# Kernel optimization log

Measured on AMD Instinct MI355X. Metric: run time of the kernel, lower is better.

The kernel has to match this reference:

```python
import jax, jax.numpy as jnp
import numpy as np

MODEL_DIM = 2048
N_HEADS = 16
T_MAX = 2048
LATENT = 512
DHR = 64
DK = MODEL_DIM // N_HEADS  # 128
B = 4
T = 2048


def _rope_tables(t, d):
    # pos pattern [0,0,1,1,...] matching repeat(2).reshape in source
    pos = jnp.repeat(jnp.arange(d // 2, dtype=jnp.float32), 2)
    theta = jnp.power(10000.0, -2.0 * pos / d)  # (d,)
    freq = jnp.arange(t, dtype=jnp.float32)[:, None]  # (t,1)
    ang = freq * theta[None, :]  # (t,d)
    return jnp.cos(ang), jnp.sin(ang)


def _apply_rope(x, cos, sin):
    # x: (B, nh, T, d); interleaved rotate-half: (x1,x2) -> (-x2, x1)
    b, nh, t, d = x.shape
    x2 = x.reshape(b, nh, t, d // 2, 2)
    x_rot = jnp.stack([-x2[..., 1], x2[..., 0]], axis=-1).reshape(b, nh, t, d)
    return x * cos[None, None] + x_rot * sin[None, None]


def setup_inputs() -> dict:
    key = jax.random.key(0)
    ks = jax.random.split(key, 14)
    s = 0.02
    f32 = jnp.float32
    return {
        "x": jax.random.normal(ks[0], (B, T, MODEL_DIM), dtype=f32),
        "W_down": jax.random.normal(ks[1], (MODEL_DIM, 2 * LATENT), dtype=f32) * s,
        "b_down": jnp.zeros((2 * LATENT,), dtype=f32),
        "W_uKV": jax.random.normal(ks[2], (LATENT, 2 * MODEL_DIM), dtype=f32) * s,
        "b_uKV": jnp.zeros((2 * MODEL_DIM,), dtype=f32),
        "W_uQ": jax.random.normal(ks[3], (LATENT, MODEL_DIM), dtype=f32) * s,
        "b_uQ": jnp.zeros((MODEL_DIM,), dtype=f32),
        "W_kr": jax.random.normal(ks[4], (MODEL_DIM, DHR), dtype=f32) * s,
        "b_kr": jnp.zeros((DHR,), dtype=f32),
        "W_qr": jax.random.normal(ks[5], (MODEL_DIM, DHR * N_HEADS), dtype=f32) * s,
        "b_qr": jnp.zeros((DHR * N_HEADS,), dtype=f32),
        "W_out": jax.random.normal(ks[6], (MODEL_DIM, MODEL_DIM), dtype=f32) * s,
        "b_out": jnp.zeros((MODEL_DIM,), dtype=f32),
    }


def reference(x, W_down, b_down, W_uKV, b_uKV, W_uQ, b_uQ,
              W_kr, b_kr, W_qr, b_qr, W_out, b_out):
    b, t, c = x.shape
    cos, sin = _rope_tables(T_MAX, DHR)
    cos, sin = cos[:t], sin[:t]

    # low-rank down projection -> latent for KV and latent for Q
    down = x @ W_down + b_down  # (B,T,2*LATENT)
    cKV, cq = jnp.split(down, 2, axis=-1)

    # decoupled RoPE channels
    kR = _apply_rope((x @ W_kr + b_kr)[:, None], cos, sin)  # (B,1,T,dhR)
    kR = jnp.broadcast_to(kR, (b, N_HEADS, t, DHR))
    qR = (x @ W_qr + b_qr).reshape(b, t, N_HEADS, DHR).transpose(0, 2, 1, 3)
    qR = _apply_rope(qR, cos, sin)  # (B,nh,T,dhR)

    # up-projections
    v_k = (cKV @ W_uKV + b_uKV).reshape(b, t, N_HEADS, 2 * DK).transpose(0, 2, 1, 3)
    v, k = jnp.split(v_k, 2, axis=-1)  # (B,nh,T,dk) each
    k = jnp.concatenate([k, kR], axis=-1)  # (B,nh,T,dk+dhR)
    q = (cq @ W_uQ + b_uQ).reshape(b, t, N_HEADS, DK).transpose(0, 2, 1, 3)
    q = jnp.concatenate([q, qR], axis=-1)  # (B,nh,T,dk+dhR)

    # scaled dot-product attention (unmasked, as in source; scale uses dk only)
    w = jnp.einsum('bhtd,bhsd->bhts', q, k) * (1.0 / DK ** 0.5)
    w = jax.nn.softmax(w, axis=-1)
    out = jnp.einsum('bhts,bhsd->bhtd', w, v)  # (B,nh,T,dk)
    out = out.transpose(0, 2, 1, 3).reshape(b, t, MODEL_DIM)
    return out @ W_out + b_out
```

## Files before the change

kernel.cpp:

```cpp
#include <hip/hip_runtime.h>
#include <hip/hip_bf16.h>

typedef unsigned short u16;
typedef unsigned int u32;
typedef __attribute__((ext_vector_type(4))) float f32x4;
typedef __attribute__((ext_vector_type(8))) short s16x8;

#define NHEADS 16
#define TSEQ 2048
#define BATCH 4
#define BT (BATCH*TSEQ)

__device__ __forceinline__ float bf2f(u16 v){ u32 u=((u32)v)<<16; return __builtin_bit_cast(float,u); }
__device__ __forceinline__ u16 f2bf(float f){ u32 u=__builtin_bit_cast(u32,f); u += 0x7fffu + ((u>>16)&1u); return (u16)(u>>16); }

__device__ __forceinline__ void gload16(const void* g, void* l){
  __builtin_amdgcn_global_load_lds((const __attribute__((address_space(1))) u32*)g,
                                   (__attribute__((address_space(3))) u32*)l, 16, 0, 0);
}

__global__ void cast_bf16_kernel(const float* __restrict__ in, u16* __restrict__ out, long n){
  long i = ((long)blockIdx.x*256 + threadIdx.x)*4;
  if (i >= n) return;
  float4 v = *(const float4*)(in + i);
  ushort4 o;
  o.x = f2bf(v.x); o.y = f2bf(v.y); o.z = f2bf(v.z); o.w = f2bf(v.w);
  *(ushort4*)(out + i) = o;
}

__global__ void transpose_cast_kernel(const float* __restrict__ in, u16* __restrict__ out, int R, int C){
  __shared__ float tile[32][33];
  int bc = blockIdx.x*32, br = blockIdx.y*32;
  int lx = threadIdx.x & 31, ly = threadIdx.x >> 5;
  #pragma unroll
  for (int i=0;i<32;i+=8)
    tile[ly+i][lx] = in[(long)(br+ly+i)*C + bc + lx];
  __syncthreads();
  #pragma unroll
  for (int i=0;i<32;i+=8)
    out[(long)(bc+ly+i)*R + br + lx] = f2bf(tile[lx][ly+i]);
}

__global__ void rope_tab_kernel(float* __restrict__ ctab, float* __restrict__ stab){
  int idx = blockIdx.x*256 + threadIdx.x;
  int t = idx >> 5, i = idx & 31;
  float theta = expf(-(float)i * (9.210340371976184f/32.0f));
  float ang = (float)t * theta;
  float s, c;
  sincosf(ang, &s, &c);
  ctab[idx] = c; stab[idx] = s;
}

__global__ void concat_bias_kernel(const float* __restrict__ a, const float* __restrict__ b,
                                   const float* __restrict__ c, float* __restrict__ o){
  int i = blockIdx.x*256 + threadIdx.x;
  if (i >= 2176) return;
  float v = 0.f;
  if (i < 1024) v = a[i];
  else if (i < 2048) v = b[i-1024];
  else if (i < 2112) v = c[i-2048];
  o[i] = v;
}

__global__ void rope_inplace_kernel(u32* __restrict__ buf, const float* __restrict__ ct,
                                    const float* __restrict__ st, int log2ppr, int rstride){
  long idx = (long)blockIdx.x*256 + threadIdx.x;
  long row = idx >> log2ppr;
  int pp = (int)(idx & ((1<<log2ppr)-1));
  int t = (int)(row & (TSEQ-1));
  int pr = pp & 31;
  u32* p = buf + row*(long)rstride + pp;
  u32 v = *p;
  float x0 = bf2f((u16)v), x1 = bf2f((u16)(v>>16));
  float c = ct[t*32+pr], s = st[t*32+pr];
  float y0 = x0*c - x1*s;
  float y1 = x1*c + x0*s;
  *p = (u32)f2bf(y0) | ((u32)f2bf(y1)<<16);
}

template<int OUTF32>
__global__ __launch_bounds__(256,2) void gemm_bt_kernel(
    const u16* __restrict__ A, const u16* __restrict__ Bt, const float* __restrict__ bias,
    void* __restrict__ Cp, int M, int N, int K, int lda, int ldb, int ldc)
{
  __shared__ u16 As[128*32];
  __shared__ u16 Bs[128*32];
  const int tid = threadIdx.x;
  const int lane = tid & 63;
  const int wave = tid >> 6;
  const long bm = (long)blockIdx.x * 128;
  const long bn = (long)blockIdx.y * 128;
  const int wr = (wave>>1)*64, wc = (wave&1)*64;
  const int g = lane>>4, r15 = lane&15;

  f32x4 acc[4][4];
  #pragma unroll
  for (int m=0;m<4;m++)
    #pragma unroll
    for (int n=0;n<4;n++) acc[m][n] = (f32x4){0.f,0.f,0.f,0.f};

  const int c0 = tid, c1 = tid + 256;
  const u16* gA0 = A + (bm + (c0>>2))*lda + (c0&3)*8;
  const u16* gA1 = A + (bm + (c1>>2))*lda + (c1&3)*8;
  const u16* gB0 = Bt + (bn + (c0>>2))*ldb + (c0&3)*8;
  const u16* gB1 = Bt + (bn + (c1>>2))*ldb + (c1&3)*8;
  u16* lA0 = As + c0*8;
  u16* lA1 = As + c1*8;
  u16* lB0 = Bs + c0*8;
  u16* lB1 = Bs + c1*8;

  for (int k0 = 0; k0 < K; k0 += 32) {
    __syncthreads();
    gload16(gA0 + k0, lA0);
    gload16(gA1 + k0, lA1);
    gload16(gB0 + k0, lB0);
    gload16(gB1 + k0, lB1);
    __syncthreads();
    s16x8 af[4], bfr[4];
    #pragma unroll
    for (int m=0;m<4;m++) af[m] = *(const s16x8*)(As + (wr + m*16 + r15)*32 + g*8);
    #pragma unroll
    for (int n=0;n<4;n++) bfr[n] = *(const s16x8*)(Bs + (wc + n*16 + r15)*32 + g*8);
    #pragma unroll
    for (int m=0;m<4;m++)
      #pragma unroll
      for (int n=0;n<4;n++)
        acc[m][n] = __builtin_amdgcn_mfma_f32_16x16x32_bf16(af[m], bfr[n], acc[m][n], 0,0,0);
  }

  #pragma unroll
  for (int n=0;n<4;n++){
    long col = bn + wc + n*16 + r15;
    if (col >= N) continue;
    float bv = bias[col];
    #pragma unroll
    for (int m=0;m<4;m++){
      long row0 = bm + wr + m*16 + g*4;
      #pragma unroll
      for (int i=0;i<4;i++){
        long row = row0 + i;
        if (row < M){
          float v = acc[m][n][i] + bv;
          if (OUTF32) ((float*)Cp)[row*(long)ldc + col] = v;
          else        ((u16*)Cp)[row*(long)ldc + col] = f2bf(v);
        }
      }
    }
  }
}

__global__ void transpose_v_kernel(const u16* __restrict__ vk_b, u16* __restrict__ Vt){
  __shared__ u16 tile[128][130];
  int t0 = blockIdx.x*128;
  int bh = blockIdx.y;
  int b = bh>>4, h = bh&15;
  for (int idx = threadIdx.x; idx < 128*128; idx += 256){
    int r = idx>>7, c = idx&127;
    tile[r][c] = vk_b[((long)(b*TSEQ + t0 + r))*4096 + h*256 + c];
  }
  __syncthreads();
  for (int idx = threadIdx.x; idx < 128*128; idx += 256){
    int d = idx>>7, tt = idx&127;
    Vt[((long)bh*128 + d)*TSEQ + t0 + tt] = tile[tt][d];
  }
}

__global__ __launch_bounds__(256,2) void attn_kernel(
    const u16* __restrict__ q_b, const u16* __restrict__ qrB,
    const u16* __restrict__ vk_b, const u16* __restrict__ krB,
    const u16* __restrict__ Vt, u16* __restrict__ attn_b)
{
  __shared__ u16 Ks[64*192];
  __shared__ u16 Vs[128*64];
  __shared__ u16 Ps[4][16*64];

  const int tid = threadIdx.x;
  const int lane = tid & 63;
  const int wave = tid >> 6;
  const int g = lane >> 4;
  const int r15 = lane & 15;
  const int bh = blockIdx.y;
  const int b = bh>>4, h = bh&15;
  const int q0 = blockIdx.x*64 + wave*16;

  s16x8 qf[6];
  {
    const u16* qp  = q_b + ((long)b*TSEQ + q0 + r15)*2048 + h*128 + g*8;
    const u16* qrp = qrB + ((long)b*TSEQ + q0 + r15)*2112 + h*64  + g*8;
    #pragma unroll
    for (int kd=0;kd<4;kd++) qf[kd] = *(const s16x8*)(qp + kd*32);
    qf[4] = *(const s16x8*)(qrp);
    qf[5] = *(const s16x8*)(qrp + 32);
  }

  f32x4 oacc[8];
  #pragma unroll
  for (int i=0;i<8;i++) oacc[i] = (f32x4){0.f,0.f,0.f,0.f};
  float mrow[4] = {-__builtin_inff(),-__builtin_inff(),-__builtin_inff(),-__builtin_inff()};
  float lrow[4] = {0.f,0.f,0.f,0.f};

  const int krow_s = tid>>2;
  const int kslot_s = tid&3;
  const int vrow_s = tid>>1;
  const int vslot_s = tid&1;
  const u16* kbase = vk_b + (long)b*TSEQ*4096 + h*256 + 128 + kslot_s*8;
  const u16* rbase = krB + (long)b*TSEQ*2112 + kslot_s*8;
  const long vg_base = (long)bh*128*TSEQ;
  char* KsB = (char*)Ks;
  char* VsB = (char*)Vs;
  char* PsB = (char*)(&Ps[wave][0]);

  s16x8 kreg[6], vreg[4];

  auto load_regs = [&](int kt){
    long t = (long)(kt*64 + krow_s);
    const u16* kp = kbase + t*4096;
    const u16* rp = rbase + t*2112;
    #pragma unroll
    for (int j=0;j<4;j++) kreg[j] = *(const s16x8*)(kp + j*32);
    kreg[4] = *(const s16x8*)(rp);
    kreg[5] = *(const s16x8*)(rp + 32);
    const u16* vsrc = Vt + vg_base + (long)vrow_s*TSEQ + kt*64 + vslot_s*8;
    #pragma unroll
    for (int j=0;j<4;j++) vreg[j] = *(const s16x8*)(vsrc + j*16);
  };
  auto write_lds = [&](){
    u32 base = (u32)((krow_s*24 + kslot_s)*16);
    u32 sw = (u32)((krow_s&7)<<4);
    #pragma unroll
    for (int j=0;j<6;j++)
      *(s16x8*)(KsB + ((base + j*64) ^ sw)) = kreg[j];
    u32 vbase = (u32)((vrow_s*8 + vslot_s)*16);
    u32 vsw = (u32)((vrow_s&7)<<4);
    #pragma unroll
    for (int j=0;j<4;j++)
      *(s16x8*)(VsB + ((vbase + j*32) ^ vsw)) = vreg[j];
  };

  load_regs(0);
  write_lds();
  __syncthreads();

  for (int kt=0; kt<32; ++kt) {
    if (kt < 31) load_regs(kt+1);

    f32x4 sacc[4];
    #pragma unroll
    for (int n=0;n<4;n++) sacc[n] = (f32x4){0.f,0.f,0.f,0.f};
    __builtin_amdgcn_s_setprio(1);
    #pragma unroll
    for (int kd=0; kd<6; kd++){
      #pragma unroll
      for (int n=0;n<4;n++){
        int krow = n*16 + r15;
        u32 byt = (u32)(krow*384 + kd*64 + g*16) ^ (u32)((krow&7)<<4);
        s16x8 kfr = *(const s16x8*)(KsB + byt);
        sacc[n] = __builtin_amdgcn_mfma_f32_16x16x32_bf16(qf[kd], kfr, sacc[n], 0,0,0);
      }
    }
    __builtin_amdgcn_s_setprio(0);

    const float scale = 0.08838834764831845f;
    float tmax[4];
    #pragma unroll
    for (int i=0;i<4;i++){
      float m0 = fmaxf(fmaxf(sacc[0][i],sacc[1][i]), fmaxf(sacc[2][i],sacc[3][i]));
      #pragma unroll
      for (int off=1; off<16; off<<=1) m0 = fmaxf(m0, __shfl_xor(m0, off));
      tmax[i] = m0*scale;
    }
    float grow = 0.f;
    #pragma unroll
    for (int i=0;i<4;i++) grow = fmaxf(grow, tmax[i]-mrow[i]);
    if (__any(grow > 8.0f)){
      float psc[4];
      #pragma unroll
      for (int i=0;i<4;i++){
        float mn = fmaxf(mrow[i], tmax[i]);
        psc[i] = __expf(mrow[i]-mn);
        mrow[i] = mn;
        lrow[i] *= psc[i];
      }
      #pragma unroll
      for (int nf=0;nf<8;nf++){
        f32x4 o = oacc[nf];
        o[0]*=psc[0]; o[1]*=psc[1]; o[2]*=psc[2]; o[3]*=psc[3];
        oacc[nf] = o;
      }
    }
    float rs[4] = {0.f,0.f,0.f,0.f};
    #pragma unroll
    for (int n=0;n<4;n++){
      #pragma unroll
      for (int i=0;i<4;i++){
        float p = __expf(sacc[n][i]*scale - mrow[i]);
        rs[i] += p;
        int prow = g*4+i;
        u32 pb = (u32)(prow*128 + (n*16+r15)*2) ^ (u32)((prow&7)<<4);
        *(u16*)(PsB + pb) = f2bf(p);
      }
    }
    #pragma unroll
    for (int i=0;i<4;i++){
      float rsum = rs[i];
      #pragma unroll
      for (int off=1; off<16; off<<=1) rsum += __shfl_xor(rsum, off);
      lrow[i] += rsum;
    }

    __builtin_amdgcn_s_setprio(1);
    #pragma unroll
    for (int ks=0; ks<2; ks++){
      u32 pb = (u32)(r15*128 + ks*64 + g*16) ^ (u32)((r15&7)<<4);
      s16x8 pf = *(const s16x8*)(PsB + pb);
      #pragma unroll
      for (int nf=0;nf<8;nf++){
        int vrow = nf*16 + r15;
        u32 vb = (u32)(vrow*128 + ks*64 + g*16) ^ (u32)((vrow&7)<<4);
        s16x8 vf = *(const s16x8*)(VsB + vb);
        oacc[nf] = __builtin_amdgcn_mfma_f32_16x16x32_bf16(pf, vf, oacc[nf], 0,0,0);
      }
    }
    __builtin_amdgcn_s_setprio(0);

    __syncthreads();
    if (kt < 31) write_lds();
    __syncthreads();
  }

  #pragma unroll
  for (int nf=0;nf<8;nf++){
    #pragma unroll
    for (int i=0;i<4;i++){
      float v = oacc[nf][i] / lrow[i];
      long t = q0 + g*4 + i;
      attn_b[((long)b*TSEQ + t)*2048 + h*128 + nf*16 + r15] = f2bf(v);
    }
  }
}

extern "C" void kernel_launch(void* const* d_in, const int* in_sizes, int n_in,
                              void* d_out, int out_size, void* d_ws, size_t ws_size,
                              hipStream_t stream)
{
  const float* x      = (const float*)d_in[0];
  const float* W_down = (const float*)d_in[1];
  const float* b_down = (const float*)d_in[2];
  const float* W_uKV  = (const float*)d_in[3];
  const float* b_uKV  = (const float*)d_in[4];
  const float* W_uQ   = (const float*)d_in[5];
  const float* b_uQ   = (const float*)d_in[6];
  const float* W_kr   = (const float*)d_in[7];
  const float* b_kr   = (const float*)d_in[8];
  const float* W_qr   = (const float*)d_in[9];
  const float* b_qr   = (const float*)d_in[10];
  const float* W_out  = (const float*)d_in[11];
  const float* b_out  = (const float*)d_in[12];
  float* out = (float*)d_out;

  char* ws = (char*)d_ws;
  size_t off = 0;
  auto alloc = [&](size_t b)->char* { char* p = ws + off; off += (b + 255) & ~(size_t)255; return p; };

  u16* xb     = (u16*)alloc((size_t)BT*2048*2);
  u16* attn_b = xb;
  u16* q_b    = (u16*)alloc((size_t)BT*2048*2);
  u16* vk_b   = (u16*)alloc((size_t)BT*4096*2);
  u16* C1     = (u16*)alloc((size_t)BT*2112*2);
  u16* W1_t   = (u16*)alloc((size_t)2176*2048*2);
  u16* WuKV_t = (u16*)alloc((size_t)4096*512*2);
  u16* WuQ_t  = (u16*)alloc((size_t)2048*512*2);
  u16* Wout_t = (u16*)alloc((size_t)2048*2048*2);
  float* ctab = (float*)alloc((size_t)2048*32*4);
  float* stab = (float*)alloc((size_t)2048*32*4);
  float* bias1= (float*)alloc((size_t)2176*4);
  u16* Vt     = (u16*)d_out;

  long nx = (long)BT*2048;
  cast_bf16_kernel<<<dim3((u32)(nx/4/256)), 256, 0, stream>>>(x, xb, nx);
  transpose_cast_kernel<<<dim3(32, 64), 256, 0, stream>>>(W_down, W1_t,             2048, 1024);
  transpose_cast_kernel<<<dim3(32, 64), 256, 0, stream>>>(W_qr,  W1_t + 1024*2048,  2048, 1024);
  transpose_cast_kernel<<<dim3(2, 64),  256, 0, stream>>>(W_kr,  W1_t + 2048*2048,  2048, 64);
  transpose_cast_kernel<<<dim3(128,16), 256, 0, stream>>>(W_uKV, WuKV_t, 512, 4096);
  transpose_cast_kernel<<<dim3(64, 16), 256, 0, stream>>>(W_uQ,  WuQ_t, 512, 2048);
  transpose_cast_kernel<<<dim3(64, 64), 256, 0, stream>>>(W_out, Wout_t, 2048, 2048);
  rope_tab_kernel<<<dim3(256), 256, 0, stream>>>(ctab, stab);
  concat_bias_kernel<<<dim3(9), 256, 0, stream>>>(b_down, b_qr, b_kr, bias1);

  gemm_bt_kernel<0><<<dim3(64, 17), 256, 0, stream>>>(xb, W1_t, bias1, C1, 8192, 2112, 2048, 2048, 2048, 2112);
  gemm_bt_kernel<0><<<dim3(64, 32), 256, 0, stream>>>(C1,       WuKV_t, b_uKV, vk_b, 8192, 4096, 512, 2112, 512, 4096);
  gemm_bt_kernel<0><<<dim3(64, 16), 256, 0, stream>>>(C1 + 512, WuQ_t,  b_uQ,  q_b,  8192, 2048, 512, 2112, 512, 2048);

  rope_inplace_kernel<<<dim3(16384), 256, 0, stream>>>((u32*)(C1 + 1024), ctab, stab, 9, 1056);
  rope_inplace_kernel<<<dim3(1024),  256, 0, stream>>>((u32*)(C1 + 2048), ctab, stab, 5, 1056);
  transpose_v_kernel<<<dim3(16, 64), 256, 0, stream>>>(vk_b, Vt);

  attn_kernel<<<dim3(32, 64), 256, 0, stream>>>(q_b, C1 + 1024, vk_b, C1 + 2048, Vt, attn_b);

  gemm_bt_kernel<1><<<dim3(64, 16), 256, 0, stream>>>(attn_b, Wout_t, b_out, out, 8192, 2048, 2048, 2048, 2048, 2048);
}
```

Before: 900.7 us.

## Switch attention to 32x32x16 MFMA with 32-row query tiles per wave

The attention kernel now uses 32x32x16 bf16 MFMA instead of 16x16x32, and each wave handles 32 query rows instead of 16. The block therefore covers 128 queries and the grid is halved. This halves K/V tile reloads from global and LDS per query and gives fewer, larger MFMA issues. The cost is more registers (16-row softmax state, f32x16 accumulators), which may reduce occupancy under launch_bounds(256,2), and the grid is halved to 1024 blocks.

```diff
diff --git a/kernel.cpp b/kernel.cpp
--- a/kernel.cpp
+++ b/kernel.cpp
@@ -4,6 +4,7 @@
 typedef unsigned short u16;
 typedef unsigned int u32;
 typedef __attribute__((ext_vector_type(4))) float f32x4;
+typedef __attribute__((ext_vector_type(16))) float f32x16;
 typedef __attribute__((ext_vector_type(8))) short s16x8;
 
 #define NHEADS 16
@@ -172,32 +173,35 @@
 {
   __shared__ u16 Ks[64*192];
   __shared__ u16 Vs[128*64];
-  __shared__ u16 Ps[4][16*64];
+  __shared__ u16 Ps[4][32*64];
 
   const int tid = threadIdx.x;
   const int lane = tid & 63;
   const int wave = tid >> 6;
-  const int g = lane >> 4;
-  const int r15 = lane & 15;
+  const int hi = lane >> 5;
+  const int r31 = lane & 31;
   const int bh = blockIdx.y;
   const int b = bh>>4, h = bh&15;
-  const int q0 = blockIdx.x*64 + wave*16;
-
-  s16x8 qf[6];
+  const int q0 = blockIdx.x*128 + wave*32;
+
+  s16x8 qf[12];
   {
-    const u16* qp  = q_b + ((long)b*TSEQ + q0 + r15)*2048 + h*128 + g*8;
-    const u16* qrp = qrB + ((long)b*TSEQ + q0 + r15)*2112 + h*64  + g*8;
-    #pragma unroll
-    for (int kd=0;kd<4;kd++) qf[kd] = *(const s16x8*)(qp + kd*32);
-    qf[4] = *(const s16x8*)(qrp);
-    qf[5] = *(const s16x8*)(qrp + 32);
-  }
-
-  f32x4 oacc[8];
-  #pragma unroll
-  for (int i=0;i<8;i++) oacc[i] = (f32x4){0.f,0.f,0.f,0.f};
-  float mrow[4] = {-__builtin_inff(),-__builtin_inff(),-__builtin_inff(),-__builtin_inff()};
-  float lrow[4] = {0.f,0.f,0.f,0.f};
+    const u16* qp  = q_b + ((long)b*TSEQ + q0 + r31)*2048 + h*128 + hi*8;
+    const u16* qrp = qrB + ((long)b*TSEQ + q0 + r31)*2112 + h*64  + hi*8;
+    #pragma unroll
+    for (int kd=0;kd<8;kd++)  qf[kd] = *(const s16x8*)(qp + kd*16);
+    #pragma unroll
+    for (int kd=8;kd<12;kd++) qf[kd] = *(const s16x8*)(qrp + (kd-8)*16);
+  }
+
+  f32x16 oacc[4];
+  #pragma unroll
+  for (int n=0;n<4;n++)
+    #pragma unroll
+    for (int r=0;r<16;r++) oacc[n][r] = 0.f;
+  float mrow[16], lrow[16];
+  #pragma unroll
+  for (int r=0;r<16;r++){ mrow[r] = -__builtin_inff(); lrow[r] = 0.f; }
 
   const int krow_s = tid>>2;
   const int kslot_s = tid&3;
@@ -244,81 +248,78 @@
   for (int kt=0; kt<32; ++kt) {
     if (kt < 31) load_regs(kt+1);
 
-    f32x4 sacc[4];
-    #pragma unroll
-    for (int n=0;n<4;n++) sacc[n] = (f32x4){0.f,0.f,0.f,0.f};
+    f32x16 sacc0, sacc1;
+    #pragma unroll
+    for (int r=0;r<16;r++){ sacc0[r]=0.f; sacc1[r]=0.f; }
     __builtin_amdgcn_s_setprio(1);
     #pragma unroll
-    for (int kd=0; kd<6; kd++){
+    for (int kd=0; kd<12; kd++){
+      u32 row0 = (u32)r31;
+      u32 byt0 = (row0*384u + (u32)(kd*32) + (u32)(hi*16)) ^ ((row0&7u)<<4);
+      s16x8 kfr0 = *(const s16x8*)(KsB + byt0);
+      sacc0 = __builtin_amdgcn_mfma_f32_32x32x16_bf16(qf[kd], kfr0, sacc0, 0,0,0);
+      u32 row1 = (u32)(32 + r31);
+      u32 byt1 = (row1*384u + (u32)(kd*32) + (u32)(hi*16)) ^ ((row1&7u)<<4);
+      s16x8 kfr1 = *(const s16x8*)(KsB + byt1);
+      sacc1 = __builtin_amdgcn_mfma_f32_32x32x16_bf16(qf[kd], kfr1, sacc1, 0,0,0);
+    }
+    __builtin_amdgcn_s_setprio(0);
+
+    const float scale = 0.08838834764831845f;
+    float tmax[16];
+    #pragma unroll
+    for (int r=0;r<16;r++){
+      float m0 = fmaxf(sacc0[r], sacc1[r]);
+      #pragma unroll
+      for (int off=1; off<32; off<<=1) m0 = fmaxf(m0, __shfl_xor(m0, off));
+      tmax[r] = m0*scale;
+    }
+    float grow = 0.f;
+    #pragma unroll
+    for (int r=0;r<16;r++) grow = fmaxf(grow, tmax[r]-mrow[r]);
+    if (__any(grow > 8.0f)){
+      #pragma unroll
+      for (int r=0;r<16;r++){
+        float mn = fmaxf(mrow[r], tmax[r]);
+        float psc = __expf(mrow[r]-mn);
+        mrow[r] = mn;
+        lrow[r] *= psc;
+        #pragma unroll
+        for (int n=0;n<4;n++) oacc[n][r] *= psc;
+      }
+    }
+    float rs[16];
+    #pragma unroll
+    for (int r=0;r<16;r++){
+      int qrow = (r&3) + 8*(r>>2) + 4*hi;
+      u32 sw = ((u32)qrow&7u)<<4;
+      float p0 = __expf(sacc0[r]*scale - mrow[r]);
+      float p1 = __expf(sacc1[r]*scale - mrow[r]);
+      rs[r] = p0 + p1;
+      u32 pb0 = ((u32)(qrow*128 + r31*2)) ^ sw;
+      u32 pb1 = ((u32)(qrow*128 + 64 + r31*2)) ^ sw;
+      *(u16*)(PsB + pb0) = f2bf(p0);
+      *(u16*)(PsB + pb1) = f2bf(p1);
+    }
+    #pragma unroll
+    for (int r=0;r<16;r++){
+      float rsum = rs[r];
+      #pragma unroll
+      for (int off=1; off<32; off<<=1) rsum += __shfl_xor(rsum, off);
+      lrow[r] += rsum;
+    }
+
+    __builtin_amdgcn_s_setprio(1);
+    #pragma unroll
+    for (int ks=0; ks<4; ks++){
+      u32 pb = ((u32)(r31*128 + ks*32 + hi*16)) ^ (((u32)r31&7u)<<4);
+      s16x8 pf = *(const s16x8*)(PsB + pb);
       #pragma unroll
       for (int n=0;n<4;n++){
-        int krow = n*16 + r15;
-        u32 byt = (u32)(krow*384 + kd*64 + g*16) ^ (u32)((krow&7)<<4);
-        s16x8 kfr = *(const s16x8*)(KsB + byt);
-        sacc[n] = __builtin_amdgcn_mfma_f32_16x16x32_bf16(qf[kd], kfr, sacc[n], 0,0,0);
-      }
-    }
-    __builtin_amdgcn_s_setprio(0);
-
-    const float scale = 0.08838834764831845f;
-    float tmax[4];
-    #pragma unroll
-    for (int i=0;i<4;i++){
-      float m0 = fmaxf(fmaxf(sacc[0][i],sacc[1][i]), fmaxf(sacc[2][i],sacc[3][i]));
-      #pragma unroll
-      for (int off=1; off<16; off<<=1) m0 = fmaxf(m0, __shfl_xor(m0, off));
-      tmax[i] = m0*scale;
-    }
-    float grow = 0.f;
-    #pragma unroll
-    for (int i=0;i<4;i++) grow = fmaxf(grow, tmax[i]-mrow[i]);
-    if (__any(grow > 8.0f)){
-      float psc[4];
-      #pragma unroll
-      for (int i=0;i<4;i++){
-        float mn = fmaxf(mrow[i], tmax[i]);
-        psc[i] = __expf(mrow[i]-mn);
-        mrow[i] = mn;
-        lrow[i] *= psc[i];
-      }
-      #pragma unroll
-      for (int nf=0;nf<8;nf++){
-        f32x4 o = oacc[nf];
-        o[0]*=psc[0]; o[1]*=psc[1]; o[2]*=psc[2]; o[3]*=psc[3];
-        oacc[nf] = o;
-      }
-    }
-    float rs[4] = {0.f,0.f,0.f,0.f};
-    #pragma unroll
-    for (int n=0;n<4;n++){
-      #pragma unroll
-      for (int i=0;i<4;i++){
-        float p = __expf(sacc[n][i]*scale - mrow[i]);
-        rs[i] += p;
-        int prow = g*4+i;
-        u32 pb = (u32)(prow*128 + (n*16+r15)*2) ^ (u32)((prow&7)<<4);
-        *(u16*)(PsB + pb) = f2bf(p);
-      }
-    }
-    #pragma unroll
-    for (int i=0;i<4;i++){
-      float rsum = rs[i];
-      #pragma unroll
-      for (int off=1; off<16; off<<=1) rsum += __shfl_xor(rsum, off);
-      lrow[i] += rsum;
-    }
-
-    __builtin_amdgcn_s_setprio(1);
-    #pragma unroll
-    for (int ks=0; ks<2; ks++){
-      u32 pb = (u32)(r15*128 + ks*64 + g*16) ^ (u32)((r15&7)<<4);
-      s16x8 pf = *(const s16x8*)(PsB + pb);
-      #pragma unroll
-      for (int nf=0;nf<8;nf++){
-        int vrow = nf*16 + r15;
-        u32 vb = (u32)(vrow*128 + ks*64 + g*16) ^ (u32)((vrow&7)<<4);
+        u32 vrow = (u32)(n*32 + r31);
+        u32 vb = (vrow*128u + (u32)(ks*32 + hi*16)) ^ ((vrow&7u)<<4);
         s16x8 vf = *(const s16x8*)(VsB + vb);
-        oacc[nf] = __builtin_amdgcn_mfma_f32_16x16x32_bf16(pf, vf, oacc[nf], 0,0,0);
+        oacc[n] = __builtin_amdgcn_mfma_f32_32x32x16_bf16(pf, vf, oacc[n], 0,0,0);
       }
     }
     __builtin_amdgcn_s_setprio(0);
@@ -329,12 +330,13 @@
   }
 
   #pragma unroll
-  for (int nf=0;nf<8;nf++){
-    #pragma unroll
-    for (int i=0;i<4;i++){
-      float v = oacc[nf][i] / lrow[i];
-      long t = q0 + g*4 + i;
-      attn_b[((long)b*TSEQ + t)*2048 + h*128 + nf*16 + r15] = f2bf(v);
+  for (int n=0;n<4;n++){
+    #pragma unroll
+    for (int r=0;r<16;r++){
+      int qrow = (r&3) + 8*(r>>2) + 4*hi;
+      float v = oacc[n][r] / lrow[r];
+      long t = q0 + qrow;
+      attn_b[((long)b*TSEQ + t)*2048 + h*128 + n*32 + r31] = f2bf(v);
     }
   }
 }
@@ -395,7 +397,7 @@
   rope_inplace_kernel<<<dim3(1024),  256, 0, stream>>>((u32*)(C1 + 2048), ctab, stab, 5, 1056);
   transpose_v_kernel<<<dim3(16, 64), 256, 0, stream>>>(vk_b, Vt);
 
-  attn_kernel<<<dim3(32, 64), 256, 0, stream>>>(q_b, C1 + 1024, vk_b, C1 + 2048, Vt, attn_b);
+  attn_kernel<<<dim3(16, 64), 256, 0, stream>>>(q_b, C1 + 1024, vk_b, C1 + 2048, Vt, attn_b);
 
   gemm_bt_kernel<1><<<dim3(64, 16), 256, 0, stream>>>(attn_b, Wout_t, b_out, out, 8192, 2048, 2048, 2048, 2048, 2048);
 }
```

Result: slower. 1.682 ms (+86.8%).
